# Performance work log

Hardware: AMD Instinct MI355X
Metric: run time of the kernel (lower is better)

The kernel has to match this reference:

```python
import jax, jax.numpy as jnp
import numpy as np

B, N, H, NH, HD, DE = 4, 512, 512, 8, 64, 64
DFF = 4 * H
EPS = 1e-5


def setup_inputs() -> dict:
    key = jax.random.key(0)
    ks = jax.random.split(key, 32)
    w = lambda k, *s: jax.random.normal(k, s, jnp.float32) * 0.02
    inp = {}
    inp['messages'] = jax.random.normal(ks[0], (B, N, H), jnp.float32)
    inp['distance_matrix'] = jax.random.randint(ks[1], (B, N, N), 0, 201).astype(jnp.float32)
    mask = jax.random.randint(ks[2], (B, N, N), 0, 2).astype(jnp.float32)
    inp['mask'] = jnp.maximum(mask, jnp.eye(N, dtype=jnp.float32)[None])  # ensure diag visible
    inp['emb_table'] = w(ks[3], 201, DE)
    inp['Wdq'] = w(ks[4], H, DE); inp['bdq'] = jnp.zeros((H,), jnp.float32)
    inp['Wdk'] = w(ks[5], H, DE); inp['bdk'] = jnp.zeros((H,), jnp.float32)
    inp['Wq'] = w(ks[6], H, H);   inp['bq'] = jnp.zeros((H,), jnp.float32)
    inp['Wk'] = w(ks[7], H, H);   inp['bk'] = jnp.zeros((H,), jnp.float32)
    inp['Wv'] = w(ks[8], H, H);   inp['bv'] = jnp.zeros((H,), jnp.float32)
    inp['Wo'] = w(ks[9], H, H);   inp['bo'] = jnp.zeros((H,), jnp.float32)
    inp['W_ih'] = w(ks[10], 3 * H, H); inp['b_ih'] = jnp.zeros((3 * H,), jnp.float32)
    inp['W_hh'] = w(ks[11], 3 * H, H); inp['b_hh'] = jnp.zeros((3 * H,), jnp.float32)
    inp['W1'] = w(ks[12], DFF, H); inp['b1'] = jnp.zeros((DFF,), jnp.float32)
    inp['W2'] = w(ks[13], H, DFF); inp['b2'] = jnp.zeros((H,), jnp.float32)
    inp['g2'] = jnp.ones((H,), jnp.float32); inp['beta2'] = jnp.zeros((H,), jnp.float32)
    return inp


def reference(messages, distance_matrix, mask, emb_table, Wdq, bdq, Wdk, bdk,
              Wq, bq, Wk, bk, Wv, bv, Wo, bo, W_ih, b_ih, W_hh, b_hh,
              W1, b1, W2, b2, g2, beta2):
    # distance embedding lookup (B,N,N,DE)
    idx = jnp.clip(distance_matrix.astype(jnp.int32), 0, 200)
    emb = emb_table[idx]
    # mean over dim then linear == linear then mean (linear maps commute with mean)
    dq = jnp.mean(emb, axis=2) @ Wdq.T + bdq  # (B,N,H)
    dk = jnp.mean(emb, axis=1) @ Wdk.T + bdk  # (B,N,H)
    Q = ((messages + dq) @ Wq.T + bq).reshape(B, N, NH, HD).transpose(0, 2, 1, 3)
    K = ((messages + dk) @ Wk.T + bk).reshape(B, N, NH, HD).transpose(0, 2, 1, 3)
    V = (messages @ Wv.T + bv).reshape(B, N, NH, HD).transpose(0, 2, 1, 3)
    scale = 1.0 / np.sqrt(HD).astype(np.float32)
    scores = jnp.einsum('bhnd,bhmd->bhnm', Q, K) * scale
    scores = jnp.where(mask[:, None] == 0, -jnp.inf, scores)
    aw = jax.nn.softmax(scores, axis=-1)
    ao = jnp.einsum('bhnm,bhmd->bhnd', aw, V).transpose(0, 2, 1, 3).reshape(B, N, H)
    ao = ao @ Wo.T + bo
    # GRUCell: x = attn output, h = messages
    gx = ao @ W_ih.T + b_ih
    gh = messages @ W_hh.T + b_hh
    xr, xz, xn = jnp.split(gx, 3, axis=-1)
    hr, hz, hn = jnp.split(gh, 3, axis=-1)
    r = jax.nn.sigmoid(xr + hr)
    z = jax.nn.sigmoid(xz + hz)
    n = jnp.tanh(xn + r * hn)
    u = (1.0 - z) * n + z * messages
    # FFN + residual + LayerNorm
    f = jax.nn.relu(u @ W1.T + b1) @ W2.T + b2
    y = u + f
    mu = jnp.mean(y, axis=-1, keepdims=True)
    var = jnp.var(y, axis=-1, keepdims=True)
    return (y - mu) / jnp.sqrt(var + EPS) * g2 + beta2
```

## Files before the change

### kernel.cpp

```cpp
#include <hip/hip_runtime.h>
#include <hip/hip_bf16.h>
#include <math.h>

#define Bz 4
#define Nn 512
#define Hh 512
#define NHh 8
#define HDd 64
#define DEe 64
#define DFFf 2048
#define EPSs 1e-5f
#define QS 1536
#define GS 3072

typedef __attribute__((ext_vector_type(8))) short bf16x8;
typedef __attribute__((ext_vector_type(4))) short bf16x4;
typedef __attribute__((ext_vector_type(4))) float f32x4;

__device__ inline short f2bf(float x) {
    unsigned u = __builtin_bit_cast(unsigned, x);
    unsigned r = (u + 0x7FFFu + ((u >> 16) & 1u)) >> 16;
    return (short)r;
}
__device__ inline float b2f(unsigned short u) {
    unsigned v = ((unsigned)u) << 16;
    return __builtin_bit_cast(float, v);
}
__device__ inline void gld16(const void* g, void* l) {
    __builtin_amdgcn_global_load_lds(
        (const __attribute__((address_space(1))) void*)g,
        (__attribute__((address_space(3))) void*)l, 16, 0, 0);
}

struct CvtSeg { const float* src; unsigned short* dst; int n, ncols, pitch; };
struct PrepArgs {
    CvtSeg cs[12];
    const float* emb; unsigned short* embb;
    const float* dist;
    unsigned short* AQ; unsigned short* AK;
    const float* Wo; unsigned short* woT;
    const float* fW[3]; const float* fv[3]; const float* fb[3]; float* fo[3];
};

__global__ __launch_bounds__(256) void prep_kernel(PrepArgs a)
{
    __shared__ char lds[17408];
    int t = threadIdx.x;
    int blk = blockIdx.x;
    if (blk < 512) {
        for (int sg = 0; sg < 12; ++sg) {
            CvtSeg c = a.cs[sg];
            int n4 = c.n >> 2;
            for (int i = blk * 256 + t; i < n4; i += 512 * 256) {
                int base = i * 4;
                int row = base / c.ncols;
                int col = base - row * c.ncols;
                float4 v = *(const float4*)(c.src + base);
                ushort4 o = {(unsigned short)f2bf(v.x), (unsigned short)f2bf(v.y),
                             (unsigned short)f2bf(v.z), (unsigned short)f2bf(v.w)};
                *(ushort4*)(c.dst + (size_t)row * c.pitch + col) = o;
            }
        }
        const float sc = 1.0f / 512.0f;
        for (int i = blk * 256 + t; i < 4096; i += 512 * 256) {
            ushort4 o = {0, 0, 0, 0};
            if (i * 4 < 201 * 64) {
                float4 v = *(const float4*)(a.emb + i * 4);
                o.x = (unsigned short)f2bf(v.x * sc);
                o.y = (unsigned short)f2bf(v.y * sc);
                o.z = (unsigned short)f2bf(v.z * sc);
                o.w = (unsigned short)f2bf(v.w * sc);
            }
            *(ushort4*)(a.embb + i * 4) = o;
        }
    } else if (blk < 552) {
        int fid = blk - 512;
        int f, ob;
        if (fid < 8)       { f = 0; ob = fid * 64; }
        else if (fid < 16) { f = 1; ob = (fid - 8) * 64; }
        else               { f = 2; ob = (fid - 16) * 64; }
        int i = ob + (t >> 2), part = t & 3;
        const float* Wr = a.fW[f] + (size_t)i * 512 + part * 128;
        const float* vv = a.fv[f] + part * 128;
        float s = 0.f;
        for (int k = 0; k < 128; k += 4) {
            float4 w4 = *(const float4*)(Wr + k);
            float4 b4 = *(const float4*)(vv + k);
            s += w4.x * b4.x + w4.y * b4.y + w4.z * b4.z + w4.w * b4.w;
        }
        s += __shfl_xor(s, 1);
        s += __shfl_xor(s, 2);
        if (part == 0) a.fo[f][i] = a.fb[f][i] + s;
    } else if (blk < 616) {
        int tid = blk - 552;
        int ti = tid >> 3, tj = tid & 7;
        float (*T)[68] = (float (*)[68])lds;
        int rr = t >> 4, c4 = (t & 15) * 4;
#pragma unroll
        for (int p = 0; p < 4; ++p) {
            int r = rr + p * 16;
            float4 v = *(const float4*)(a.Wo + (size_t)(ti * 64 + r) * 512 + tj * 64 + c4);
            *(float4*)&T[r][c4] = v;
        }
        __syncthreads();
#pragma unroll
        for (int p = 0; p < 4; ++p) {
            int jr = rr + p * 16;
            ushort4 o = {(unsigned short)f2bf(T[c4 + 0][jr]),
                         (unsigned short)f2bf(T[c4 + 1][jr]),
                         (unsigned short)f2bf(T[c4 + 2][jr]),
                         (unsigned short)f2bf(T[c4 + 3][jr])};
            *(ushort4*)(a.woT + (size_t)(tj * 64 + jr) * 512 + ti * 64 + c4) = o;
        }
    } else if (blk < 2664) {
        int r = blk - 616;
        int* hist = (int*)lds;
        hist[t] = 0;
        __syncthreads();
        float2 v = *(const float2*)(a.dist + (size_t)r * 512 + t * 2);
        atomicAdd(&hist[min(max((int)v.x, 0), 200)], 1);
        atomicAdd(&hist[min(max((int)v.y, 0), 200)], 1);
        __syncthreads();
        a.AQ[(size_t)r * 768 + 512 + t] = (unsigned short)f2bf((float)hist[t]);
    } else {
        int idx = blk - 2664;
        int b = idx >> 5, jt = idx & 31;
        int j0 = jt * 16;
        int* h2 = (int*)lds;
        for (int k = t; k < 4096; k += 256) h2[k] = 0;
        __syncthreads();
        int ri = t >> 4, jj = t & 15;
        for (int i0 = 0; i0 < 512; i0 += 16) {
            float v = a.dist[(size_t)(b * 512 + i0 + ri) * 512 + j0 + jj];
            atomicAdd(&h2[jj * 256 + min(max((int)v, 0), 200)], 1);
        }
        __syncthreads();
        for (int k = t; k < 4096; k += 256) {
            int jj2 = k >> 8, bin = k & 255;
            a.AK[(size_t)(b * 512 + j0 + jj2) * 768 + 512 + bin] =
                (unsigned short)f2bf((float)h2[k]);
        }
    }
}

struct Seg {
    const unsigned short* A; const unsigned short* W;
    const float* bias; const void* res; void* C;
    int lda, Ks, ldw, rlda, ldc, pad;
};
struct SegArgs { Seg s[6]; };

template<int BM, int BN, int RELU, int RESM, int OUTF, int HASB>
__global__ __launch_bounds__(256) void mgf_kernel(SegArgs sa, int SW)
{
    constexpr int WM = BM / 2, WN = BN / 2;
    constexpr int MT = WM / 16, NT = WN / 16;
    constexpr int IPA = BM / 32, IPB = BN / 32;
    __shared__ unsigned short As[2][BM * 64];
    __shared__ unsigned short Bs[2][BN * 64];
    int t = threadIdx.x, lane = t & 63, wid = t >> 6;
    int wm = wid >> 1, wn = wid & 1;
    int m0 = blockIdx.y * BM, n0 = blockIdx.x * BN;
    int seg = n0 / SW;
    const unsigned short* A = sa.s[seg].A;
    const unsigned short* W = sa.s[seg].W;
    int lda = sa.s[seg].lda, Ks = sa.s[seg].Ks, ldw = sa.s[seg].ldw;
    int nloc = n0 - seg * SW;
    int lrow8 = lane >> 3;
    int lunit = (lane & 7) ^ lrow8;

    f32x4 acc[MT][NT] = {};

    auto stage = [&](int buf, int kt) {
#pragma unroll
        for (int i = 0; i < IPA; ++i) {
            int c = wid * IPA + i;
            gld16(A + (size_t)(m0 + c * 8 + lrow8) * lda + kt + lunit * 8,
                  &As[buf][c * 512]);
        }
#pragma unroll
        for (int i = 0; i < IPB; ++i) {
            int c = wid * IPB + i;
            gld16(W + (size_t)(nloc + c * 8 + lrow8) * ldw + kt + lunit * 8,
                  &Bs[buf][c * 512]);
        }
    };

    stage(0, 0);
    __syncthreads();
    int cur = 0;
    for (int kt = 0; kt < Ks; kt += 64) {
        if (kt + 64 < Ks) stage(cur ^ 1, kt + 64);
#pragma unroll
        for (int kk = 0; kk < 2; ++kk) {
            bf16x8 fa[MT], fb[NT];
            int ub = kk * 4 + (lane >> 4);
#pragma unroll
            for (int mt = 0; mt < MT; ++mt) {
                int r = wm * WM + mt * 16 + (lane & 15);
                fa[mt] = *(const bf16x8*)&As[cur][r * 64 + ((ub ^ (r & 7)) << 3)];
            }
#pragma unroll
            for (int nt = 0; nt < NT; ++nt) {
                int r = wn * WN + nt * 16 + (lane & 15);
                fb[nt] = *(const bf16x8*)&Bs[cur][r * 64 + ((ub ^ (r & 7)) << 3)];
            }
#pragma unroll
            for (int mt = 0; mt < MT; ++mt)
#pragma unroll
                for (int nt = 0; nt < NT; ++nt)
                    acc[mt][nt] = __builtin_amdgcn_mfma_f32_16x16x32_bf16(
                        fa[mt], fb[nt], acc[mt][nt], 0, 0, 0);
        }
        __syncthreads();
        cur ^= 1;
    }

    int cr = (lane >> 4) * 4, ccl = lane & 15;
    const float* bias = sa.s[seg].bias;
    const void* res = sa.s[seg].res;
    int rlda = sa.s[seg].rlda, ldc = sa.s[seg].ldc;
    void* C = sa.s[seg].C;
#pragma unroll
    for (int mt = 0; mt < MT; ++mt) {
#pragma unroll
        for (int nt = 0; nt < NT; ++nt) {
            int lcol = nloc + wn * WN + nt * 16 + ccl;
            float bv = HASB ? bias[lcol] : 0.f;
#pragma unroll
            for (int r = 0; r < 4; ++r) {
                int row = m0 + wm * WM + mt * 16 + cr + r;
                float o = acc[mt][nt][r] + bv;
                if (RESM == 1)
                    o += ((const float*)res)[(size_t)row * rlda + lcol];
                if (RESM == 2)
                    o += b2f(((const unsigned short*)res)[(size_t)row * rlda + lcol]);
                if (RELU) o = fmaxf(o, 0.f);
                if (OUTF)
                    ((float*)C)[(size_t)row * ldc + lcol] = o;
                else
                    ((unsigned short*)C)[(size_t)row * ldc + lcol] =
                        (unsigned short)f2bf(o);
            }
        }
    }
}

__global__ __launch_bounds__(256) void attn_mfma_kernel(
    const unsigned short* __restrict__ QKV, const float* __restrict__ mask,
    unsigned short* __restrict__ AO)
{
    __shared__ unsigned short Qs[64 * 64];
    __shared__ unsigned short Ks[64 * 64];
    __shared__ unsigned short Vt[64 * 64];
    __shared__ float Ms[64 * 65];
    __shared__ unsigned short Pl[4][16 * 72];

    int t = threadIdx.x;
    int lane = t & 63;
    int wq = t >> 6;
    int g = lane >> 4, cc = lane & 15;
    int q0 = blockIdx.x * 64;
    int h = blockIdx.y, b = blockIdx.z;

    int lr = t >> 2;
    int u0 = (t & 3) * 2;
    int c0f = (t & 3) * 16;

    {
        const unsigned short* src =
            QKV + ((size_t)(b * Nn + q0 + lr)) * QS + h * HDd + u0 * 8;
        bf16x8 p0 = *(const bf16x8*)(src);
        bf16x8 p1 = *(const bf16x8*)(src + 8);
        *(bf16x8*)&Qs[lr * 64 + ((u0 ^ (lr & 7)) << 3)] = p0;
        *(bf16x8*)&Qs[lr * 64 + (((u0 + 1) ^ (lr & 7)) << 3)] = p1;
    }

    const unsigned short* Krow =
        QKV + ((size_t)(b * Nn + lr)) * QS + 512 + h * HDd + u0 * 8;
    int vkey = t >> 4;
    int vd0 = (t & 15) * 4;
    const unsigned short* Vbase =
        QKV + ((size_t)(b * Nn)) * QS + 1024 + h * HDd + vd0;
    const float* Mrow = mask + ((size_t)(b * Nn + q0 + lr)) * Nn + c0f;

    bf16x8 kr0, kr1;
    ushort4 vr[4];
    float4 mreg[4];
    auto issue = [&](int kc) {
        int k0 = kc * 64;
        const unsigned short* kp = Krow + (size_t)k0 * QS;
        kr0 = *(const bf16x8*)(kp);
        kr1 = *(const bf16x8*)(kp + 8);
        const float* mp = Mrow + k0;
        mreg[0] = *(const float4*)(mp);
        mreg[1] = *(const float4*)(mp + 4);
        mreg[2] = *(const float4*)(mp + 8);
        mreg[3] = *(const float4*)(mp + 12);
#pragma unroll
        for (int p = 0; p < 4; ++p)
            vr[p] = *(const ushort4*)(Vbase + (size_t)(k0 + vkey + p * 16) * QS);
    };
    issue(0);
    __syncthreads();

    bf16x8 qf0 = *(bf16x8*)&Qs[(wq * 16 + cc) * 64 + (((0 * 4 + g) ^ (cc & 7)) << 3)];
    bf16x8 qf1 = *(bf16x8*)&Qs[(wq * 16 + cc) * 64 + (((1 * 4 + g) ^ (cc & 7)) << 3)];

    const float scale = 0.125f;
    float m_run = -1e30f, l_run = 0.f;
    f32x4 o[4] = {};

    for (int kc = 0; kc < 8; ++kc) {
        {
            *(bf16x8*)&Ks[lr * 64 + ((u0 ^ (lr & 7)) << 3)] = kr0;
            *(bf16x8*)&Ks[lr * 64 + (((u0 + 1) ^ (lr & 7)) << 3)] = kr1;

            float* msr = &Ms[lr * 65 + c0f];
            msr[0] = mreg[0].x;  msr[1] = mreg[0].y;  msr[2] = mreg[0].z;  msr[3] = mreg[0].w;
            msr[4] = mreg[1].x;  msr[5] = mreg[1].y;  msr[6] = mreg[1].z;  msr[7] = mreg[1].w;
            msr[8] = mreg[2].x;  msr[9] = mreg[2].y;  msr[10] = mreg[2].z; msr[11] = mreg[2].w;
            msr[12] = mreg[3].x; msr[13] = mreg[3].y; msr[14] = mreg[3].z; msr[15] = mreg[3].w;

#pragma unroll
            for (int p = 0; p < 4; ++p) {
                int key = vkey + p * 16;
                unsigned short vals[4] = {vr[p].x, vr[p].y, vr[p].z, vr[p].w};
#pragma unroll
                for (int jj = 0; jj < 4; ++jj) {
                    int j = (jj + (t >> 2)) & 3;
                    int d = vd0 + j;
                    Vt[d * 64 + (key ^ ((d & 7) << 3))] = vals[j];
                }
            }
        }
        __syncthreads();
        if (kc < 7) issue(kc + 1);

        f32x4 s[4] = {};
        __builtin_amdgcn_s_setprio(1);
#pragma unroll
        for (int kt = 0; kt < 4; ++kt) {
            int rA = kt * 16 + cc;
            bf16x8 a0 = *(bf16x8*)&Ks[rA * 64 + (((0 * 4 + g) ^ (rA & 7)) << 3)];
            s[kt] = __builtin_amdgcn_mfma_f32_16x16x32_bf16(a0, qf0, s[kt], 0, 0, 0);
            bf16x8 a1 = *(bf16x8*)&Ks[rA * 64 + (((1 * 4 + g) ^ (rA & 7)) << 3)];
            s[kt] = __builtin_amdgcn_mfma_f32_16x16x32_bf16(a1, qf1, s[kt], 0, 0, 0);
        }
        __builtin_amdgcn_s_setprio(0);

        float pv[4][4];
        float tmax = -1e30f;
#pragma unroll
        for (int kt = 0; kt < 4; ++kt) {
#pragma unroll
            for (int r = 0; r < 4; ++r) {
                float mv = Ms[(wq * 16 + cc) * 65 + kt * 16 + g * 4 + r];
                float svv = (mv == 0.f) ? -1e30f : s[kt][r];
                pv[kt][r] = svv;
                tmax = fmaxf(tmax, svv);
            }
        }
        tmax = fmaxf(tmax, __shfl_xor(tmax, 16));
        tmax = fmaxf(tmax, __shfl_xor(tmax, 32));
        float mnew = fmaxf(m_run, tmax);
        float rescale = __expf((m_run - mnew) * scale);
        float psum = 0.f;
#pragma unroll
        for (int kt = 0; kt < 4; ++kt) {
#pragma unroll
            for (int r = 0; r < 4; ++r) {
                float sv = pv[kt][r];
                float p = (sv == -1e30f) ? 0.f : __expf((sv - mnew) * scale);
                pv[kt][r] = p;
                psum += p;
            }
        }
        psum += __shfl_xor(psum, 16);
        psum += __shfl_xor(psum, 32);
        l_run = l_run * rescale + psum;
        m_run = mnew;
#pragma unroll
        for (int dt = 0; dt < 4; ++dt) {
            o[dt][0] *= rescale; o[dt][1] *= rescale;
            o[dt][2] *= rescale; o[dt][3] *= rescale;
        }

#pragma unroll
        for (int kt = 0; kt < 4; ++kt) {
            bf16x4 pk = {f2bf(pv[kt][0]), f2bf(pv[kt][1]),
                         f2bf(pv[kt][2]), f2bf(pv[kt][3])};
            *(bf16x4*)&Pl[wq][cc * 72 + kt * 16 + g * 4] = pk;
        }
        bf16x8 pf0 = *(bf16x8*)&Pl[wq][cc * 72 + 0 + g * 8];
        bf16x8 pf1 = *(bf16x8*)&Pl[wq][cc * 72 + 32 + g * 8];

        __builtin_amdgcn_s_setprio(1);
#pragma unroll
        for (int dt = 0; dt < 4; ++dt) {
            int rV = dt * 16 + cc;
            bf16x8 vf0 = *(bf16x8*)&Vt[rV * 64 + (((0 * 4 + g) ^ (rV & 7)) << 3)];
            o[dt] = __builtin_amdgcn_mfma_f32_16x16x32_bf16(vf0, pf0, o[dt], 0, 0, 0);
            bf16x8 vf1 = *(bf16x8*)&Vt[rV * 64 + (((1 * 4 + g) ^ (rV & 7)) << 3)];
            o[dt] = __builtin_amdgcn_mfma_f32_16x16x32_bf16(vf1, pf1, o[dt], 0, 0, 0);
        }
        __builtin_amdgcn_s_setprio(0);
        __syncthreads();
    }

    float invl = 1.f / l_run;
#pragma unroll
    for (int dt = 0; dt < 4; ++dt) {
        ushort4 w = {(unsigned short)f2bf(o[dt][0] * invl),
                     (unsigned short)f2bf(o[dt][1] * invl),
                     (unsigned short)f2bf(o[dt][2] * invl),
                     (unsigned short)f2bf(o[dt][3] * invl)};
        *(ushort4*)&AO[((size_t)(b * Nn + q0 + wq * 16 + cc)) * Hh +
                       h * HDd + dt * 16 + g * 4] = w;
    }
}

__global__ __launch_bounds__(256) void gru_kernel(
    const unsigned short* __restrict__ G,
    const float* __restrict__ msg, unsigned short* __restrict__ u)
{
    int i4 = blockIdx.x * 256 + threadIdx.x;
    int e = i4 * 4;
    int row = e >> 9, col = e & 511;
    const unsigned short* gxr = G + (size_t)row * GS;
    const unsigned short* ghr = gxr + 1536;
    ushort4 xr4 = *(const ushort4*)(gxr + col);
    ushort4 xz4 = *(const ushort4*)(gxr + col + 512);
    ushort4 xn4 = *(const ushort4*)(gxr + col + 1024);
    ushort4 hr4 = *(const ushort4*)(ghr + col);
    ushort4 hz4 = *(const ushort4*)(ghr + col + 512);
    ushort4 hn4 = *(const ushort4*)(ghr + col + 1024);
    float4 mg4 = *(const float4*)(msg + e);
    float mv[4] = {mg4.x, mg4.y, mg4.z, mg4.w};
    unsigned short xr[4] = {xr4.x, xr4.y, xr4.z, xr4.w};
    unsigned short xz[4] = {xz4.x, xz4.y, xz4.z, xz4.w};
    unsigned short xn[4] = {xn4.x, xn4.y, xn4.z, xn4.w};
    unsigned short hr[4] = {hr4.x, hr4.y, hr4.z, hr4.w};
    unsigned short hz[4] = {hz4.x, hz4.y, hz4.z, hz4.w};
    unsigned short hn[4] = {hn4.x, hn4.y, hn4.z, hn4.w};
    ushort4 out;
    unsigned short* op = (unsigned short*)&out;
#pragma unroll
    for (int j = 0; j < 4; ++j) {
        float r = 1.f / (1.f + __expf(-(b2f(xr[j]) + b2f(hr[j]))));
        float z = 1.f / (1.f + __expf(-(b2f(xz[j]) + b2f(hz[j]))));
        float n = tanhf(b2f(xn[j]) + r * b2f(hn[j]));
        op[j] = (unsigned short)f2bf((1.f - z) * n + z * mv[j]);
    }
    *(ushort4*)(u + e) = out;
}

__global__ __launch_bounds__(256) void ln_kernel(
    const float* __restrict__ Y, const float* __restrict__ g,
    const float* __restrict__ be, float* __restrict__ out)
{
    int row = blockIdx.x, t = threadIdx.x;
    const float* yr = Y + (size_t)row * Hh;
    float v0 = yr[t], v1 = yr[t + 256];
    float s = v0 + v1, s2 = v0 * v0 + v1 * v1;
#pragma unroll
    for (int o = 1; o < 64; o <<= 1) {
        s += __shfl_xor(s, o);
        s2 += __shfl_xor(s2, o);
    }
    __shared__ float rs[4], rs2[4];
    int w = t >> 6;
    if ((t & 63) == 0) { rs[w] = s; rs2[w] = s2; }
    __syncthreads();
    float ts = rs[0] + rs[1] + rs[2] + rs[3];
    float ts2 = rs2[0] + rs2[1] + rs2[2] + rs2[3];
    float mu = ts * (1.0f / Hh);
    float var = ts2 * (1.0f / Hh) - mu * mu;
    float rstd = rsqrtf(var + EPSs);
    out[(size_t)row * Hh + t] = (v0 - mu) * rstd * g[t] + be[t];
    out[(size_t)row * Hh + t + 256] = (v1 - mu) * rstd * g[t + 256] + be[t + 256];
}

extern "C" void kernel_launch(void* const* d_in, const int* in_sizes, int n_in,
                              void* d_out, int out_size, void* d_ws, size_t ws_size,
                              hipStream_t stream) {
    const float* messages = (const float*)d_in[0];
    const float* dist     = (const float*)d_in[1];
    const float* mask     = (const float*)d_in[2];
    const float* emb      = (const float*)d_in[3];
    const float* Wdq = (const float*)d_in[4];  const float* bdq = (const float*)d_in[5];
    const float* Wdk = (const float*)d_in[6];  const float* bdk = (const float*)d_in[7];
    const float* Wq  = (const float*)d_in[8];  const float* bq  = (const float*)d_in[9];
    const float* Wk  = (const float*)d_in[10]; const float* bk  = (const float*)d_in[11];
    const float* Wv  = (const float*)d_in[12]; const float* bv  = (const float*)d_in[13];
    const float* Wo  = (const float*)d_in[14]; const float* bo  = (const float*)d_in[15];
    const float* W_ih = (const float*)d_in[16]; const float* b_ih = (const float*)d_in[17];
    const float* W_hh = (const float*)d_in[18]; const float* b_hh = (const float*)d_in[19];
    const float* W1  = (const float*)d_in[20]; const float* b1  = (const float*)d_in[21];
    const float* W2  = (const float*)d_in[22]; const float* b2  = (const float*)d_in[23];
    const float* g2  = (const float*)d_in[24]; const float* beta2 = (const float*)d_in[25];

    const int M = Bz * Nn;
    char* ws = (char*)d_ws;

    unsigned short* wdqb  = (unsigned short*)(ws + 0);
    unsigned short* wdkb  = (unsigned short*)(ws + 65536);
    unsigned short* Wbigq = (unsigned short*)(ws + 131072);
    unsigned short* Wbigk = (unsigned short*)(ws + 917504);
    unsigned short* wvb   = (unsigned short*)(ws + 1703936);
    unsigned short* wihb  = (unsigned short*)(ws + 2228224);
    unsigned short* whhb  = (unsigned short*)(ws + 3801088);
    unsigned short* w1b   = (unsigned short*)(ws + 5373952);
    unsigned short* w2b   = (unsigned short*)(ws + 7471104);
    unsigned short* msgs  = (unsigned short*)(ws + 9568256);
    unsigned short* AQ    = (unsigned short*)(ws + 11665408);
    unsigned short* AK    = (unsigned short*)(ws + 14811136);
    unsigned short* embb  = (unsigned short*)(ws + 17956864);
    unsigned short* EcatT = (unsigned short*)(ws + 17989632);
    unsigned short* woT   = (unsigned short*)(ws + 18513920);
    unsigned short* Wfih  = (unsigned short*)(ws + 19038208);
    unsigned short* QKVb  = (unsigned short*)(ws + 20611072);
    unsigned short* AO    = (unsigned short*)(ws + 26902528);
    unsigned short* G     = (unsigned short*)(ws + 28999680);
    unsigned short* ub    = (unsigned short*)(ws + 41582592);
    unsigned short* f1    = (unsigned short*)(ws + 43679744);
    float*          yb    = (float*)(ws + 52068352);
    float*          bqp   = (float*)(ws + 56262656);
    float*          bkp   = (float*)(ws + 56264704);
    float*          bgxp  = (float*)(ws + 56266752);

    dim3 blk(256);

    PrepArgs pa;
    pa.cs[0]  = {messages, msgs,  M * Hh,        512, 512};
    pa.cs[1]  = {messages, AQ,    M * Hh,        512, 768};
    pa.cs[2]  = {messages, AK,    M * Hh,        512, 768};
    pa.cs[3]  = {Wdq,      wdqb,  Hh * DEe,      64,  64};
    pa.cs[4]  = {Wdk,      wdkb,  Hh * DEe,      64,  64};
    pa.cs[5]  = {Wq,       Wbigq, Hh * Hh,       512, 768};
    pa.cs[6]  = {Wk,       Wbigk, Hh * Hh,       512, 768};
    pa.cs[7]  = {Wv,       wvb,   Hh * Hh,       512, 512};
    pa.cs[8]  = {W_ih,     wihb,  3 * Hh * Hh,   512, 512};
    pa.cs[9]  = {W_hh,     whhb,  3 * Hh * Hh,   512, 512};
    pa.cs[10] = {W1,       w1b,   DFFf * Hh,     512, 512};
    pa.cs[11] = {W2,       w2b,   Hh * DFFf,     2048, 2048};
    pa.emb = emb; pa.embb = embb;
    pa.dist = dist; pa.AQ = AQ; pa.AK = AK;
    pa.Wo = Wo; pa.woT = woT;
    pa.fW[0] = Wq;   pa.fv[0] = bdq; pa.fb[0] = bq;   pa.fo[0] = bqp;
    pa.fW[1] = Wk;   pa.fv[1] = bdk; pa.fb[1] = bk;   pa.fo[1] = bkp;
    pa.fW[2] = W_ih; pa.fv[2] = bo;  pa.fb[2] = b_ih; pa.fo[2] = bgxp;
    prep_kernel<<<2792, blk, 0, stream>>>(pa);

    {
        SegArgs sa = {};
        sa.s[0] = {embb, wdqb, nullptr, nullptr, EcatT, 64, 64, 64, 0, 1024, 0};
        mgf_kernel<64, 128, 0, 0, 0, 0><<<dim3(8, 4), blk, 0, stream>>>(sa, 1024);
    }

    {
        SegArgs sa = {};
        sa.s[0] = {Wbigq, EcatT,       nullptr, nullptr, Wbigq + 512, 768, 512, 1024, 0, 768, 0};
        sa.s[1] = {Wbigk, EcatT + 512, nullptr, nullptr, Wbigk + 512, 768, 512, 1024, 0, 768, 0};
        mgf_kernel<64, 64, 0, 0, 0, 0><<<dim3(8, 8), blk, 0, stream>>>(sa, 256);
    }

    {
        SegArgs sa = {};
        sa.s[0] = {wihb, woT, nullptr, nullptr, Wfih, 512, 512, 512, 0, 512, 0};
        mgf_kernel<64, 128, 0, 0, 0, 0><<<dim3(4, 24), blk, 0, stream>>>(sa, 512);
    }

    {
        SegArgs sa = {};
        sa.s[0] = {AQ,   Wbigq,             bqp,          nullptr, QKVb,        768, 768, 768, 0, QS, 0};
        sa.s[1] = {AK,   Wbigk,             bkp,          nullptr, QKVb + 512,  768, 768, 768, 0, QS, 0};
        sa.s[2] = {msgs, wvb,               bv,           nullptr, QKVb + 1024, 512, 512, 512, 0, QS, 0};
        sa.s[3] = {msgs, whhb,              b_hh,         nullptr, G + 1536,    512, 512, 512, 0, GS, 0};
        sa.s[4] = {msgs, whhb + 512 * 512,  b_hh + 512,   nullptr, G + 2048,    512, 512, 512, 0, GS, 0};
        sa.s[5] = {msgs, whhb + 1024 * 512, b_hh + 1024,  nullptr, G + 2560,    512, 512, 512, 0, GS, 0};
        mgf_kernel<64, 128, 0, 0, 0, 1><<<dim3(24, 32), blk, 0, stream>>>(sa, 512);
    }

    attn_mfma_kernel<<<dim3(Nn / 64, NHh, Bz), blk, 0, stream>>>(QKVb, mask, AO);

    {
        SegArgs sa = {};
        sa.s[0] = {AO, Wfih, bgxp, nullptr, G, 512, 512, 512, 0, GS, 0};
        mgf_kernel<64, 128, 0, 0, 0, 1><<<dim3(12, 32), blk, 0, stream>>>(sa, 1536);
    }

    gru_kernel<<<(M * Hh) / 1024, blk, 0, stream>>>(G, messages, ub);

    {
        SegArgs sa = {};
        sa.s[0] = {ub, w1b, b1, nullptr, f1, 512, 512, 512, 0, DFFf, 0};
        mgf_kernel<64, 128, 1, 0, 0, 1><<<dim3(16, 32), blk, 0, stream>>>(sa, 2048);
    }
    {
        SegArgs sa = {};
        sa.s[0] = {f1, w2b, b2, ub, yb, 2048, 2048, 2048, 512, 512, 0};
        mgf_kernel<64, 64, 0, 2, 1, 1><<<dim3(8, 32), blk, 0, stream>>>(sa, 512);
    }

    ln_kernel<<<M, blk, 0, stream>>>(yb, g2, beta2, (float*)d_out);
}
```

Measured before the change: 124.9 us.

## Bit-pack attention mask, split-K GEMM sources, merge small weight GEMMs

```diff
diff --git a/kernel.cpp b/kernel.cpp
--- a/kernel.cpp
+++ b/kernel.cpp
@@ -34,11 +34,12 @@
 
 struct CvtSeg { const float* src; unsigned short* dst; int n, ncols, pitch; };
 struct PrepArgs {
-    CvtSeg cs[12];
+    CvtSeg cs[10];
     const float* emb; unsigned short* embb;
     const float* dist;
-    unsigned short* AQ; unsigned short* AK;
+    unsigned short* histq; unsigned short* histk;
     const float* Wo; unsigned short* woT;
+    const float* mask; unsigned long long* mbits;
     const float* fW[3]; const float* fv[3]; const float* fb[3]; float* fo[3];
 };
 
@@ -48,7 +49,7 @@
     int t = threadIdx.x;
     int blk = blockIdx.x;
     if (blk < 512) {
-        for (int sg = 0; sg < 12; ++sg) {
+        for (int sg = 0; sg < 10; ++sg) {
             CvtSeg c = a.cs[sg];
             int n4 = c.n >> 2;
             for (int i = blk * 256 + t; i < n4; i += 512 * 256) {
@@ -121,8 +122,8 @@
         atomicAdd(&hist[min(max((int)v.x, 0), 200)], 1);
         atomicAdd(&hist[min(max((int)v.y, 0), 200)], 1);
         __syncthreads();
-        a.AQ[(size_t)r * 768 + 512 + t] = (unsigned short)f2bf((float)hist[t]);
-    } else {
+        a.histq[(size_t)r * 256 + t] = (unsigned short)f2bf((float)hist[t]);
+    } else if (blk < 2792) {
         int idx = blk - 2664;
         int b = idx >> 5, jt = idx & 31;
         int j0 = jt * 16;
@@ -137,16 +138,28 @@
         __syncthreads();
         for (int k = t; k < 4096; k += 256) {
             int jj2 = k >> 8, bin = k & 255;
-            a.AK[(size_t)(b * 512 + j0 + jj2) * 768 + 512 + bin] =
+            a.histk[(size_t)(b * 512 + j0 + jj2) * 256 + bin] =
                 (unsigned short)f2bf((float)h2[k]);
         }
+    } else {
+        int idx = blk - 2792;
+        int wv = t >> 6, lane = t & 63;
+#pragma unroll
+        for (int i = 0; i < 16; ++i) {
+            int word = (idx * 4 + wv) * 16 + i;
+            int rowg = word >> 3, w = word & 7;
+            float mv = a.mask[(size_t)rowg * 512 + w * 64 + lane];
+            unsigned long long bits = __ballot(mv != 0.0f);
+            if (lane == 0) a.mbits[word] = bits;
+        }
     }
 }
 
 struct Seg {
-    const unsigned short* A; const unsigned short* W;
+    const unsigned short* A; const unsigned short* A2;
+    const unsigned short* W;
     const float* bias; const void* res; void* C;
-    int lda, Ks, ldw, rlda, ldc, pad;
+    int lda, lda2, ksplit, Ks, ldw, rlda, ldc, Ms;
 };
 struct SegArgs { Seg s[6]; };
 
@@ -162,9 +175,12 @@
     int wm = wid >> 1, wn = wid & 1;
     int m0 = blockIdx.y * BM, n0 = blockIdx.x * BN;
     int seg = n0 / SW;
+    if (m0 >= sa.s[seg].Ms) return;
     const unsigned short* A = sa.s[seg].A;
+    const unsigned short* A2 = sa.s[seg].A2;
     const unsigned short* W = sa.s[seg].W;
-    int lda = sa.s[seg].lda, Ks = sa.s[seg].Ks, ldw = sa.s[seg].ldw;
+    int lda = sa.s[seg].lda, lda2 = sa.s[seg].lda2, ksplit = sa.s[seg].ksplit;
+    int Ks = sa.s[seg].Ks, ldw = sa.s[seg].ldw;
     int nloc = n0 - seg * SW;
     int lrow8 = lane >> 3;
     int lunit = (lane & 7) ^ lrow8;
@@ -172,10 +188,14 @@
     f32x4 acc[MT][NT] = {};
 
     auto stage = [&](int buf, int kt) {
+        const unsigned short* Asrc;
+        int koff, ldaa;
+        if (kt < ksplit) { Asrc = A; koff = kt; ldaa = lda; }
+        else             { Asrc = A2; koff = kt - ksplit; ldaa = lda2; }
 #pragma unroll
         for (int i = 0; i < IPA; ++i) {
             int c = wid * IPA + i;
-            gld16(A + (size_t)(m0 + c * 8 + lrow8) * lda + kt + lunit * 8,
+            gld16(Asrc + (size_t)(m0 + c * 8 + lrow8) * ldaa + koff + lunit * 8,
                   &As[buf][c * 512]);
         }
 #pragma unroll
@@ -247,13 +267,13 @@
 }
 
 __global__ __launch_bounds__(256) void attn_mfma_kernel(
-    const unsigned short* __restrict__ QKV, const float* __restrict__ mask,
+    const unsigned short* __restrict__ QKV,
+    const unsigned long long* __restrict__ mbits,
     unsigned short* __restrict__ AO)
 {
     __shared__ unsigned short Qs[64 * 64];
     __shared__ unsigned short Ks[64 * 64];
     __shared__ unsigned short Vt[64 * 64];
-    __shared__ float Ms[64 * 65];
     __shared__ unsigned short Pl[4][16 * 72];
 
     int t = threadIdx.x;
@@ -265,7 +285,6 @@
 
     int lr = t >> 2;
     int u0 = (t & 3) * 2;
-    int c0f = (t & 3) * 16;
 
     {
         const unsigned short* src =
@@ -282,21 +301,16 @@
     int vd0 = (t & 15) * 4;
     const unsigned short* Vbase =
         QKV + ((size_t)(b * Nn)) * QS + 1024 + h * HDd + vd0;
-    const float* Mrow = mask + ((size_t)(b * Nn + q0 + lr)) * Nn + c0f;
+    const unsigned long long* Mb =
+        mbits + ((size_t)(b * Nn + q0 + wq * 16 + cc)) * 8;
 
     bf16x8 kr0, kr1;
     ushort4 vr[4];
-    float4 mreg[4];
     auto issue = [&](int kc) {
         int k0 = kc * 64;
         const unsigned short* kp = Krow + (size_t)k0 * QS;
         kr0 = *(const bf16x8*)(kp);
         kr1 = *(const bf16x8*)(kp + 8);
-        const float* mp = Mrow + k0;
-        mreg[0] = *(const float4*)(mp);
-        mreg[1] = *(const float4*)(mp + 4);
-        mreg[2] = *(const float4*)(mp + 8);
-        mreg[3] = *(const float4*)(mp + 12);
 #pragma unroll
         for (int p = 0; p < 4; ++p)
             vr[p] = *(const ushort4*)(Vbase + (size_t)(k0 + vkey + p * 16) * QS);
@@ -315,13 +329,6 @@
         {
             *(bf16x8*)&Ks[lr * 64 + ((u0 ^ (lr & 7)) << 3)] = kr0;
             *(bf16x8*)&Ks[lr * 64 + (((u0 + 1) ^ (lr & 7)) << 3)] = kr1;
-
-            float* msr = &Ms[lr * 65 + c0f];
-            msr[0] = mreg[0].x;  msr[1] = mreg[0].y;  msr[2] = mreg[0].z;  msr[3] = mreg[0].w;
-            msr[4] = mreg[1].x;  msr[5] = mreg[1].y;  msr[6] = mreg[1].z;  msr[7] = mreg[1].w;
-            msr[8] = mreg[2].x;  msr[9] = mreg[2].y;  msr[10] = mreg[2].z; msr[11] = mreg[2].w;
-            msr[12] = mreg[3].x; msr[13] = mreg[3].y; msr[14] = mreg[3].z; msr[15] = mreg[3].w;
-
 #pragma unroll
             for (int p = 0; p < 4; ++p) {
                 int key = vkey + p * 16;
@@ -334,6 +341,7 @@
                 }
             }
         }
+        unsigned long long mw = Mb[kc];
         __syncthreads();
         if (kc < 7) issue(kc + 1);
 
@@ -355,8 +363,8 @@
         for (int kt = 0; kt < 4; ++kt) {
 #pragma unroll
             for (int r = 0; r < 4; ++r) {
-                float mv = Ms[(wq * 16 + cc) * 65 + kt * 16 + g * 4 + r];
-                float svv = (mv == 0.f) ? -1e30f : s[kt][r];
+                int kpos = kt * 16 + g * 4 + r;
+                float svv = ((mw >> kpos) & 1ull) ? s[kt][r] : -1e30f;
                 pv[kt][r] = svv;
                 tmax = fmaxf(tmax, svv);
             }
@@ -513,93 +521,104 @@
     unsigned short* w1b   = (unsigned short*)(ws + 5373952);
     unsigned short* w2b   = (unsigned short*)(ws + 7471104);
     unsigned short* msgs  = (unsigned short*)(ws + 9568256);
-    unsigned short* AQ    = (unsigned short*)(ws + 11665408);
-    unsigned short* AK    = (unsigned short*)(ws + 14811136);
-    unsigned short* embb  = (unsigned short*)(ws + 17956864);
-    unsigned short* EcatT = (unsigned short*)(ws + 17989632);
-    unsigned short* woT   = (unsigned short*)(ws + 18513920);
-    unsigned short* Wfih  = (unsigned short*)(ws + 19038208);
-    unsigned short* QKVb  = (unsigned short*)(ws + 20611072);
-    unsigned short* AO    = (unsigned short*)(ws + 26902528);
-    unsigned short* G     = (unsigned short*)(ws + 28999680);
-    unsigned short* ub    = (unsigned short*)(ws + 41582592);
-    unsigned short* f1    = (unsigned short*)(ws + 43679744);
-    float*          yb    = (float*)(ws + 52068352);
-    float*          bqp   = (float*)(ws + 56262656);
-    float*          bkp   = (float*)(ws + 56264704);
-    float*          bgxp  = (float*)(ws + 56266752);
+    unsigned short* histq = (unsigned short*)(ws + 11665408);
+    unsigned short* histk = (unsigned short*)(ws + 12713984);
+    unsigned short* embb  = (unsigned short*)(ws + 13762560);
+    unsigned short* EcatTq= (unsigned short*)(ws + 13795328);
+    unsigned short* EcatTk= (unsigned short*)(ws + 14057472);
+    unsigned short* woT   = (unsigned short*)(ws + 14319616);
+    unsigned short* Wfih  = (unsigned short*)(ws + 14843904);
+    unsigned short* QKVb  = (unsigned short*)(ws + 16416768);
+    unsigned short* AO    = (unsigned short*)(ws + 22708224);
+    unsigned short* G     = (unsigned short*)(ws + 24805376);
+    unsigned short* ub    = (unsigned short*)(ws + 37388288);
+    unsigned short* f1    = (unsigned short*)(ws + 39485440);
+    float*          yb    = (float*)(ws + 47874048);
+    float*          bqp   = (float*)(ws + 52068352);
+    float*          bkp   = (float*)(ws + 52070400);
+    float*          bgxp  = (float*)(ws + 52072448);
+    unsigned long long* mbits = (unsigned long long*)(ws + 52078592);
 
     dim3 blk(256);
 
     PrepArgs pa;
-    pa.cs[0]  = {messages, msgs,  M * Hh,        512, 512};
-    pa.cs[1]  = {messages, AQ,    M * Hh,        512, 768};
-    pa.cs[2]  = {messages, AK,    M * Hh,        512, 768};
-    pa.cs[3]  = {Wdq,      wdqb,  Hh * DEe,      64,  64};
-    pa.cs[4]  = {Wdk,      wdkb,  Hh * DEe,      64,  64};
-    pa.cs[5]  = {Wq,       Wbigq, Hh * Hh,       512, 768};
-    pa.cs[6]  = {Wk,       Wbigk, Hh * Hh,       512, 768};
-    pa.cs[7]  = {Wv,       wvb,   Hh * Hh,       512, 512};
-    pa.cs[8]  = {W_ih,     wihb,  3 * Hh * Hh,   512, 512};
-    pa.cs[9]  = {W_hh,     whhb,  3 * Hh * Hh,   512, 512};
-    pa.cs[10] = {W1,       w1b,   DFFf * Hh,     512, 512};
-    pa.cs[11] = {W2,       w2b,   Hh * DFFf,     2048, 2048};
+    pa.cs[0] = {messages, msgs,  M * Hh,      512,  512};
+    pa.cs[1] = {Wdq,      wdqb,  Hh * DEe,    64,   64};
+    pa.cs[2] = {Wdk,      wdkb,  Hh * DEe,    64,   64};
+    pa.cs[3] = {Wq,       Wbigq, Hh * Hh,     512,  768};
+    pa.cs[4] = {Wk,       Wbigk, Hh * Hh,     512,  768};
+    pa.cs[5] = {Wv,       wvb,   Hh * Hh,     512,  512};
+    pa.cs[6] = {W_ih,     wihb,  3 * Hh * Hh, 512,  512};
+    pa.cs[7] = {W_hh,     whhb,  3 * Hh * Hh, 512,  512};
+    pa.cs[8] = {W1,       w1b,   DFFf * Hh,   512,  512};
+    pa.cs[9] = {W2,       w2b,   Hh * DFFf,   2048, 2048};
     pa.emb = emb; pa.embb = embb;
-    pa.dist = dist; pa.AQ = AQ; pa.AK = AK;
+    pa.dist = dist; pa.histq = histq; pa.histk = histk;
     pa.Wo = Wo; pa.woT = woT;
+    pa.mask = mask; pa.mbits = mbits;
     pa.fW[0] = Wq;   pa.fv[0] = bdq; pa.fb[0] = bq;   pa.fo[0] = bqp;
     pa.fW[1] = Wk;   pa.fv[1] = bdk; pa.fb[1] = bk;   pa.fo[1] = bkp;
     pa.fW[2] = W_ih; pa.fv[2] = bo;  pa.fb[2] = b_ih; pa.fo[2] = bgxp;
-    prep_kernel<<<2792, blk, 0, stream>>>(pa);
+    prep_kernel<<<3048, blk, 0, stream>>>(pa);
 
     {
         SegArgs sa = {};
-        sa.s[0] = {embb, wdqb, nullptr, nullptr, EcatT, 64, 64, 64, 0, 1024, 0};
-        mgf_kernel<64, 128, 0, 0, 0, 0><<<dim3(8, 4), blk, 0, stream>>>(sa, 1024);
+        sa.s[0] = {embb, nullptr, wdqb, nullptr, nullptr, EcatTq,
+                   64, 0, 9999, 64, 64, 0, 512, 256};
+        sa.s[1] = {embb, nullptr, wdkb, nullptr, nullptr, EcatTk,
+                   64, 0, 9999, 64, 64, 0, 512, 256};
+        sa.s[2] = {wihb, nullptr, woT, nullptr, nullptr, Wfih,
+                   512, 0, 9999, 512, 512, 0, 512, 1536};
+        mgf_kernel<64, 64, 0, 0, 0, 0><<<dim3(24, 24), blk, 0, stream>>>(sa, 512);
     }
 
     {
         SegArgs sa = {};
-        sa.s[0] = {Wbigq, EcatT,       nullptr, nullptr, Wbigq + 512, 768, 512, 1024, 0, 768, 0};
-        sa.s[1] = {Wbigk, EcatT + 512, nullptr, nullptr, Wbigk + 512, 768, 512, 1024, 0, 768, 0};
+        sa.s[0] = {Wbigq, nullptr, EcatTq, nullptr, nullptr, Wbigq + 512,
+                   768, 0, 9999, 512, 512, 0, 768, 512};
+        sa.s[1] = {Wbigk, nullptr, EcatTk, nullptr, nullptr, Wbigk + 512,
+                   768, 0, 9999, 512, 512, 0, 768, 512};
         mgf_kernel<64, 64, 0, 0, 0, 0><<<dim3(8, 8), blk, 0, stream>>>(sa, 256);
     }
 
     {
         SegArgs sa = {};
-        sa.s[0] = {wihb, woT, nullptr, nullptr, Wfih, 512, 512, 512, 0, 512, 0};
-        mgf_kernel<64, 128, 0, 0, 0, 0><<<dim3(4, 24), blk, 0, stream>>>(sa, 512);
-    }
+        sa.s[0] = {msgs, histq, Wbigq,             bqp,         nullptr, QKVb,
+                   512, 256, 512, 768, 768, 0, QS, 2048};
+        sa.s[1] = {msgs, histk, Wbigk,             bkp,         nullptr, QKVb + 512,
+                   512, 256, 512, 768, 768, 0, QS, 2048};
+        sa.s[2] = {msgs, nullptr, wvb,             bv,          nullptr, QKVb + 1024,
+                   512, 0, 9999, 512, 512, 0, QS, 2048};
+        sa.s[3] = {msgs, nullptr, whhb,            b_hh,        nullptr, G + 1536,
+                   512, 0, 9999, 512, 512, 0, GS, 2048};
+        sa.s[4] = {msgs, nullptr, whhb + 512 * 512, b_hh + 512, nullptr, G + 2048,
+                   512, 0, 9999, 512, 512, 0, GS, 2048};
+        sa.s[5] = {msgs, nullptr, whhb + 1024 * 512, b_hh + 1024, nullptr, G + 2560,
+                   512, 0, 9999, 512, 512, 0, GS, 2048};
+        mgf_kernel<64, 128, 0, 0, 0, 1><<<dim3(24, 32), blk, 0, stream>>>(sa, 512);
+    }
+
+    attn_mfma_kernel<<<dim3(Nn / 64, NHh, Bz), blk, 0, stream>>>(QKVb, mbits, AO);
 
     {
         SegArgs sa = {};
-        sa.s[0] = {AQ,   Wbigq,             bqp,          nullptr, QKVb,        768, 768, 768, 0, QS, 0};
-        sa.s[1] = {AK,   Wbigk,             bkp,          nullptr, QKVb + 512,  768, 768, 768, 0, QS, 0};
-        sa.s[2] = {msgs, wvb,               bv,           nullptr, QKVb + 1024, 512, 512, 512, 0, QS, 0};
-        sa.s[3] = {msgs, whhb,              b_hh,         nullptr, G + 1536,    512, 512, 512, 0, GS, 0};
-        sa.s[4] = {msgs, whhb + 512 * 512,  b_hh + 512,   nullptr, G + 2048,    512, 512, 512, 0, GS, 0};
-        sa.s[5] = {msgs, whhb + 1024 * 512, b_hh + 1024,  nullptr, G + 2560,    512, 512, 512, 0, GS, 0};
-        mgf_kernel<64, 128, 0, 0, 0, 1><<<dim3(24, 32), blk, 0, stream>>>(sa, 512);
-    }
-
-    attn_mfma_kernel<<<dim3(Nn / 64, NHh, Bz), blk, 0, stream>>>(QKVb, mask, AO);
+        sa.s[0] = {AO, nullptr, Wfih, bgxp, nullptr, G,
+                   512, 0, 9999, 512, 512, 0, GS, 2048};
+        mgf_kernel<64, 128, 0, 0, 0, 1><<<dim3(12, 32), blk, 0, stream>>>(sa, 1536);
+    }
+
+    gru_kernel<<<(M * Hh) / 1024, blk, 0, stream>>>(G, messages, ub);
 
     {
         SegArgs sa = {};
-        sa.s[0] = {AO, Wfih, bgxp, nullptr, G, 512, 512, 512, 0, GS, 0};
-        mgf_kernel<64, 128, 0, 0, 0, 1><<<dim3(12, 32), blk, 0, stream>>>(sa, 1536);
-    }
-
-    gru_kernel<<<(M * Hh) / 1024, blk, 0, stream>>>(G, messages, ub);
-
+        sa.s[0] = {ub, nullptr, w1b, b1, nullptr, f1,
+                   512, 0, 9999, 512, 512, 0, DFFf, 2048};
+        mgf_kernel<64, 128, 1, 0, 0, 1><<<dim3(16, 32), blk, 0, stream>>>(sa, 2048);
+    }
     {
         SegArgs sa = {};
-        sa.s[0] = {ub, w1b, b1, nullptr, f1, 512, 512, 512, 0, DFFf, 0};
-        mgf_kernel<64, 128, 1, 0, 0, 1><<<dim3(16, 32), blk, 0, stream>>>(sa, 2048);
-    }
-    {
-        SegArgs sa = {};
-        sa.s[0] = {f1, w2b, b2, ub, yb, 2048, 2048, 2048, 512, 512, 0};
+        sa.s[0] = {f1, nullptr, w2b, b2, ub, yb,
+                   2048, 0, 9999, 2048, 2048, 512, 512, 2048};
         mgf_kernel<64, 64, 0, 2, 1, 1><<<dim3(8, 32), blk, 0, stream>>>(sa, 512);
     }
 
```

New measurement: 120.8 us (median of 3 runs). 3.3% less time.
